# Optimization experiments

Measured on AMD Instinct MI355X. Metric: run time of the kernel, lower is better.

Reference implementation:

```python
import jax, jax.numpy as jnp
import numpy as np

B, S, D, A = 32, 2048, 512, 256


def setup_inputs() -> dict:
    key = jax.random.key(0)
    ks = jax.random.split(key, 9)
    enc = jax.random.normal(ks[0], (B, S, D), dtype=jnp.float32)
    dec = jax.random.normal(ks[1], (B, 1, D), dtype=jnp.float32)
    prev = jax.random.uniform(ks[2], (B, S), dtype=jnp.float32)
    prev = prev / jnp.sum(prev, axis=1, keepdims=True)  # normalized prev attention
    noise = jax.random.normal(ks[3], (B, S), dtype=jnp.float32)
    W = jax.random.normal(ks[4], (A, D), dtype=jnp.float32) / np.sqrt(D)
    V = jax.random.normal(ks[5], (A, D), dtype=jnp.float32) / np.sqrt(D)
    b = jax.random.normal(ks[6], (A,), dtype=jnp.float32)
    v_w = jax.random.normal(ks[7], (1, A), dtype=jnp.float32)
    v_g = jnp.full((1,), np.sqrt(1.0 / A), dtype=jnp.float32)  # weight_norm g init
    v_bias = jax.random.normal(ks[8], (1,), dtype=jnp.float32)
    r = jnp.full((1,), -4.0, dtype=jnp.float32)
    return {"encoder_outputs": enc, "decoder_h": dec, "prev_alpha": prev,
            "noise": noise, "W": W, "V": V, "b": b, "v_w": v_w,
            "v_g": v_g, "v_bias": v_bias, "r": r}


def reference(encoder_outputs, decoder_h, prev_alpha, noise, W, V, b, v_w, v_g, v_bias, r):
    # Energy: tanh-MLP Bahdanau score with weight-normed output projection
    h = jnp.tanh(jnp.einsum('bsd,ad->bsa', encoder_outputs, W)
                 + jnp.einsum('bod,ad->boa', decoder_h, V)  # [B,1,A] broadcasts over S
                 + b)
    w_eff = v_g * v_w / jnp.linalg.norm(v_w)       # weight_norm: g * v / ||v||
    energy = jnp.einsum('bsa,oa->bso', h, w_eff)[..., 0] + v_bias[0] + r[0]  # [B,S]
    # Soft monotonic attention recurrence
    p_select = jax.nn.sigmoid(energy + noise)
    log1mp = jnp.log(jnp.clip(1.0 - p_select, 1e-10, 1.0))
    cumprod_1mp = jnp.exp(jnp.cumsum(log1mp, axis=1))  # safe_cumprod
    alpha = p_select * cumprod_1mp * jnp.cumsum(prev_alpha / cumprod_1mp, axis=1)
    # Context: enc^T @ alpha
    context = jnp.einsum('bsd,bs->bd', encoder_outputs, alpha)
    return context, alpha
```

## Files before the change

### kernel.cpp

```cpp
#include <hip/hip_runtime.h>
#include <math.h>

#define B_  32
#define S_  2048
#define D_  512
#define A_  256
#define BS_ (B_ * S_)

#define WEFF_OFF  0
#define DEC_OFF   256
#define EPART_OFF 8448
#define CTX_OFF   (8448 + BS_)

typedef _Float16 f16x8 __attribute__((ext_vector_type(8)));
typedef __fp16   fp16x2 __attribute__((ext_vector_type(2)));
typedef _Float16 half4 __attribute__((ext_vector_type(4)));
typedef float floatx4 __attribute__((ext_vector_type(4)));

__device__ __forceinline__ void glds16(const void* g, void* l) {
    __builtin_amdgcn_global_load_lds(
        (const __attribute__((address_space(1))) void*)g,
        (__attribute__((address_space(3))) void*)l, 16, 0, 0);
}

__global__ void ma_prep_kernel(const float* __restrict__ v_w,
                               const float* __restrict__ v_g,
                               const float* __restrict__ dec,
                               const float* __restrict__ V,
                               const float* __restrict__ bvec,
                               const float* __restrict__ W,
                               _Float16* __restrict__ W16,
                               float* __restrict__ ws) {
    __shared__ float sh[D_];
    const int bid = blockIdx.x, t = threadIdx.x;
    if (bid == 0) {
        float v = v_w[t];
        float sq = v * v;
        #pragma unroll
        for (int off = 32; off > 0; off >>= 1) sq += __shfl_down(sq, off, 64);
        if ((t & 63) == 0) sh[t >> 6] = sq;
        __syncthreads();
        float n2 = sh[0] + sh[1] + sh[2] + sh[3];
        ws[WEFF_OFF + t] = v_g[0] * v / sqrtf(n2);
    } else if (bid <= B_) {
        const int b = bid - 1;
        sh[t]       = dec[b * D_ + t];
        sh[t + 256] = dec[b * D_ + 256 + t];
        __syncthreads();
        const float4* Vr = (const float4*)(V + (size_t)t * D_);
        float acc = 0.f;
        #pragma unroll 4
        for (int k = 0; k < D_ / 4; ++k) {
            float4 v4 = Vr[k];
            acc = fmaf(v4.x, sh[4*k+0], acc);
            acc = fmaf(v4.y, sh[4*k+1], acc);
            acc = fmaf(v4.z, sh[4*k+2], acc);
            acc = fmaf(v4.w, sh[4*k+3], acc);
        }
        ws[DEC_OFF + b * A_ + t] = acc + bvec[t];
    } else {
        int i = (bid - (B_ + 1)) * 256 + t;
        float4 v = ((const float4*)W)[i];
        half4 h;
        h[0] = (_Float16)v.x; h[1] = (_Float16)v.y;
        h[2] = (_Float16)v.z; h[3] = (_Float16)v.w;
        ((half4*)W16)[i] = h;
    }
}

__global__ __launch_bounds__(512) void ma_energy_mfma(
        const float* __restrict__ enc,
        const _Float16* __restrict__ W16,
        const float* __restrict__ ws_in,
        float* __restrict__ energy) {
    __shared__ __align__(16) float    As[2][128 * 32];
    __shared__ __align__(16) _Float16 Bs[2][256 * 32];
    __shared__ float red[4][128];

    const int t  = threadIdx.x;
    const int bx = blockIdx.x;
    const size_t R0 = (size_t)bx * 128;
    const int batch = bx >> 4;

    const int lane = t & 63, wid = t >> 6;
    const int wm = wid >> 2, wn = wid & 3;
    const int fr = lane & 15, kq = lane >> 4;

    const int arow = t >> 3, ac = t & 7;
    const float* AgS0 = enc + (R0 + (size_t)arow) * D_ + (ac ^ (arow & 7)) * 4;
    const float* AgS1 = AgS0 + (size_t)64 * D_;
    const int brow = t >> 2, bc = t & 3;
    const _Float16* BgS0 = W16 + (size_t)brow * D_ + (bc ^ ((brow >> 1) & 3)) * 8;
    const _Float16* BgS1 = BgS0 + (size_t)128 * D_;

    const int axc0 = ((2 * kq)     ^ (fr & 7)) * 4;
    const int axc1 = ((2 * kq + 1) ^ (fr & 7)) * 4;
    const int bxo  = (kq ^ ((fr >> 1) & 3)) * 8;

    floatx4 acc[4][4];
    #pragma unroll
    for (int m = 0; m < 4; ++m)
        #pragma unroll
        for (int n = 0; n < 4; ++n) acc[m][n] = (floatx4)0.f;

    glds16(AgS0, &As[0][wid * 256]);
    glds16(AgS1, &As[0][wid * 256 + 2048]);
    glds16(BgS0, &Bs[0][wid * 512]);
    glds16(BgS1, &Bs[0][wid * 512 + 4096]);
    __syncthreads();

    #pragma unroll 1
    for (int kt = 0; kt < 16; ++kt) {
        const int cur = kt & 1;
        if (kt < 15) {
            const int nxt = cur ^ 1;
            const int ko = (kt + 1) * 32;
            glds16(AgS0 + ko, &As[nxt][wid * 256]);
            glds16(AgS1 + ko, &As[nxt][wid * 256 + 2048]);
            glds16(BgS0 + ko, &Bs[nxt][wid * 512]);
            glds16(BgS1 + ko, &Bs[nxt][wid * 512 + 4096]);
        }
        f16x8 af[4];
        #pragma unroll
        for (int m = 0; m < 4; ++m) {
            const int rbase = (wm * 64 + m * 16 + fr) * 32;
            float4 lo = *(const float4*)&As[cur][rbase + axc0];
            float4 hi = *(const float4*)&As[cur][rbase + axc1];
            union { fp16x2 h2[4]; f16x8 v; } u;
            u.h2[0] = __builtin_amdgcn_cvt_pkrtz(lo.x, lo.y);
            u.h2[1] = __builtin_amdgcn_cvt_pkrtz(lo.z, lo.w);
            u.h2[2] = __builtin_amdgcn_cvt_pkrtz(hi.x, hi.y);
            u.h2[3] = __builtin_amdgcn_cvt_pkrtz(hi.z, hi.w);
            af[m] = u.v;
        }
        f16x8 bf[4];
        #pragma unroll
        for (int n = 0; n < 4; ++n)
            bf[n] = *(const f16x8*)&Bs[cur][(wn * 64 + n * 16 + fr) * 32 + bxo];
        #pragma unroll
        for (int m = 0; m < 4; ++m)
            #pragma unroll
            for (int n = 0; n < 4; ++n)
                acc[m][n] = __builtin_amdgcn_mfma_f32_16x16x32_f16(af[m], bf[n], acc[m][n], 0, 0, 0);
        __syncthreads();
    }

    const float* weff  = ws_in + WEFF_OFF;
    const float* dterm = ws_in + DEC_OFF + batch * A_;
    float wj[4], dj[4];
    #pragma unroll
    for (int n = 0; n < 4; ++n) {
        int a = wn * 64 + n * 16 + fr;
        wj[n] = weff[a];
        dj[n] = dterm[a];
    }
    #pragma unroll
    for (int m = 0; m < 4; ++m) {
        #pragma unroll
        for (int r = 0; r < 4; ++r) {
            float v = 0.f;
            #pragma unroll
            for (int n = 0; n < 4; ++n) {
                float x = acc[m][n][r] + dj[n];
                float e = __expf(2.f * x);
                v += (1.f - 2.f / (e + 1.f)) * wj[n];
            }
            #pragma unroll
            for (int mask = 1; mask < 16; mask <<= 1)
                v += __shfl_xor(v, mask, 64);
            if (fr == 0)
                red[wn][wm * 64 + m * 16 + (kq << 2) + r] = v;
        }
    }
    __syncthreads();
    if (t < 128)
        energy[R0 + t] = red[0][t] + red[1][t] + red[2][t] + red[3][t];
}

__global__ void ma_scan_kernel(const float* __restrict__ energy,
                               const float* __restrict__ noise,
                               const float* __restrict__ prev,
                               const float* __restrict__ v_bias,
                               const float* __restrict__ r,
                               float* __restrict__ alpha_out) {
    int b = blockIdx.x, t = threadIdx.x;
    const float bias = v_bias[0] + r[0];
    int base = b * S_ + t * 8;
    float p[8], av[8], bv[8];
    #pragma unroll
    for (int i = 0; i < 8; ++i) {
        float e = energy[base + i] + bias + noise[base + i];
        float pi = 1.f / (1.f + expf(-e));
        p[i]  = pi;
        av[i] = fmaxf(1.f - pi, 1e-10f);
        bv[i] = prev[base + i];
    }
    float Ai = 1.f, Bi = 0.f;
    #pragma unroll
    for (int i = 0; i < 8; ++i) { Bi = av[i] * Bi + bv[i]; Ai *= av[i]; }
    int lane = t & 63;
    #pragma unroll
    for (int off = 1; off < 64; off <<= 1) {
        float Ap = __shfl_up(Ai, off, 64);
        float Bp = __shfl_up(Bi, off, 64);
        if (lane >= off) { Bi = Ai * Bp + Bi; Ai = Ai * Ap; }
    }
    __shared__ float wA[4], wB[4];
    int w = t >> 6;
    if (lane == 63) { wA[w] = Ai; wB[w] = Bi; }
    __syncthreads();
    float Ax = __shfl_up(Ai, 1, 64);
    float Bx = __shfl_up(Bi, 1, 64);
    if (lane == 0) { Ax = 1.f; Bx = 0.f; }
    float PwA = 1.f, PwB = 0.f;
    for (int q = 0; q < w; ++q) { PwB = wA[q] * PwB + wB[q]; PwA *= wA[q]; }
    float T = Ax * PwB + Bx;
    #pragma unroll
    for (int i = 0; i < 8; ++i) {
        T = av[i] * T + bv[i];
        alpha_out[base + i] = p[i] * T;
    }
}

__global__ void ma_ctxpart_kernel(const float* __restrict__ enc,
                                  const float* __restrict__ alpha,
                                  float* __restrict__ cpart) {
    int b = blockIdx.x, sc = blockIdx.y, t = threadIdx.x;
    const int sp = t >> 7;
    const int d4 = t & 127;
    const float4* e = (const float4*)(enc + ((size_t)b * S_ + sc * 128) * D_);
    const float* al = alpha + b * S_ + sc * 128;
    float4 acc = {0.f, 0.f, 0.f, 0.f};
    #pragma unroll 4
    for (int s = sp; s < 128; s += 2) {
        float a = al[s];
        float4 v = e[(size_t)s * 128 + d4];
        acc.x = fmaf(v.x, a, acc.x);
        acc.y = fmaf(v.y, a, acc.y);
        acc.z = fmaf(v.z, a, acc.z);
        acc.w = fmaf(v.w, a, acc.w);
    }
    __shared__ float4 sh[128];
    if (sp == 1) sh[d4] = acc;
    __syncthreads();
    if (sp == 0) {
        float4 o = sh[d4];
        acc.x += o.x; acc.y += o.y; acc.z += o.z; acc.w += o.w;
        ((float4*)(cpart + ((size_t)(sc * B_ + b)) * D_))[d4] = acc;
    }
}

__global__ void ma_ctxreduce_kernel(const float* __restrict__ cpart,
                                    float* __restrict__ ctx) {
    int b = blockIdx.x, d = threadIdx.x;
    float s = 0.f;
    #pragma unroll
    for (int q = 0; q < 16; ++q) s += cpart[((size_t)(q * B_ + b)) * D_ + d];
    ctx[b * D_ + d] = s;
}

extern "C" void kernel_launch(void* const* d_in, const int* in_sizes, int n_in,
                              void* d_out, int out_size, void* d_ws, size_t ws_size,
                              hipStream_t stream) {
    const float* enc    = (const float*)d_in[0];
    const float* dec    = (const float*)d_in[1];
    const float* prev   = (const float*)d_in[2];
    const float* noise  = (const float*)d_in[3];
    const float* W      = (const float*)d_in[4];
    const float* V      = (const float*)d_in[5];
    const float* bvec   = (const float*)d_in[6];
    const float* v_w    = (const float*)d_in[7];
    const float* v_g    = (const float*)d_in[8];
    const float* v_bias = (const float*)d_in[9];
    const float* r      = (const float*)d_in[10];

    float* out = (float*)d_out;
    float* ws  = (float*)d_ws;
    float* alpha = out + B_ * D_;
    _Float16* W16 = (_Float16*)(ws + CTX_OFF);

    ma_prep_kernel<<<1 + B_ + 128, 256, 0, stream>>>(v_w, v_g, dec, V, bvec, W, W16, ws);
    ma_energy_mfma<<<512, 512, 0, stream>>>(enc, W16, ws, ws + EPART_OFF);
    ma_scan_kernel<<<B_, 256, 0, stream>>>(ws + EPART_OFF, noise, prev, v_bias, r, alpha);
    dim3 gc(B_, 16);
    ma_ctxpart_kernel<<<gc, 256, 0, stream>>>(enc, alpha, ws + CTX_OFF);
    ma_ctxreduce_kernel<<<B_, 512, 0, stream>>>(ws + CTX_OFF, out);
}
```

Measured before the change: 77.20 us.

## Stage encoder tile through registers and store fp16 in LDS

The encoder A-tile is no longer copied fp32 straight into LDS with global_load_lds. Each thread now loads it into registers, converts it to fp16 once, and writes it to a half-size swizzled LDS buffer after the MFMA loop body. This removes the redundant per-wave fp32->fp16 conversions and halves LDS footprint and A-fragment LDS read traffic. In exchange it adds register pressure and relies on register prefetch latency being hidden behind the MFMAs instead of the async LDS DMA path.

```diff
diff --git a/kernel.cpp b/kernel.cpp
--- a/kernel.cpp
+++ b/kernel.cpp
@@ -73,7 +73,7 @@
         const _Float16* __restrict__ W16,
         const float* __restrict__ ws_in,
         float* __restrict__ energy) {
-    __shared__ __align__(16) float    As[2][128 * 32];
+    __shared__ __align__(16) _Float16 As[2][128 * 32];
     __shared__ __align__(16) _Float16 Bs[2][256 * 32];
     __shared__ float red[4][128];
 
@@ -86,16 +86,15 @@
     const int wm = wid >> 2, wn = wid & 3;
     const int fr = lane & 15, kq = lane >> 4;
 
-    const int arow = t >> 3, ac = t & 7;
-    const float* AgS0 = enc + (R0 + (size_t)arow) * D_ + (ac ^ (arow & 7)) * 4;
-    const float* AgS1 = AgS0 + (size_t)64 * D_;
+    const int ar = t >> 2, aq = t & 3;
+    const float* Ag = enc + (R0 + (size_t)ar) * D_ + aq * 8;
+    const int awc = ((aq ^ ((ar >> 1) & 3)) * 8);
+
     const int brow = t >> 2, bc = t & 3;
     const _Float16* BgS0 = W16 + (size_t)brow * D_ + (bc ^ ((brow >> 1) & 3)) * 8;
     const _Float16* BgS1 = BgS0 + (size_t)128 * D_;
 
-    const int axc0 = ((2 * kq)     ^ (fr & 7)) * 4;
-    const int axc1 = ((2 * kq + 1) ^ (fr & 7)) * 4;
-    const int bxo  = (kq ^ ((fr >> 1) & 3)) * 8;
+    const int fxo = (kq ^ ((fr >> 1) & 3)) * 8;
 
     floatx4 acc[4][4];
     #pragma unroll
@@ -103,47 +102,57 @@
         #pragma unroll
         for (int n = 0; n < 4; ++n) acc[m][n] = (floatx4)0.f;
 
-    glds16(AgS0, &As[0][wid * 256]);
-    glds16(AgS1, &As[0][wid * 256 + 2048]);
-    glds16(BgS0, &Bs[0][wid * 512]);
-    glds16(BgS1, &Bs[0][wid * 512 + 4096]);
+    float4 pa0, pa1;
+
+#define LOADA(kt) do { \
+        pa0 = *(const float4*)(Ag + (kt) * 32); \
+        pa1 = *(const float4*)(Ag + (kt) * 32 + 4); \
+    } while (0)
+
+#define STOREA(buf) do { \
+        union { fp16x2 h2[4]; f16x8 v; } u; \
+        u.h2[0] = __builtin_amdgcn_cvt_pkrtz(pa0.x, pa0.y); \
+        u.h2[1] = __builtin_amdgcn_cvt_pkrtz(pa0.z, pa0.w); \
+        u.h2[2] = __builtin_amdgcn_cvt_pkrtz(pa1.x, pa1.y); \
+        u.h2[3] = __builtin_amdgcn_cvt_pkrtz(pa1.z, pa1.w); \
+        *(f16x8*)&As[buf][ar * 32 + awc] = u.v; \
+    } while (0)
+
+#define STAGEB(kt, buf) do { \
+        glds16(BgS0 + (kt) * 32, &Bs[buf][t * 8]); \
+        glds16(BgS1 + (kt) * 32, &Bs[buf][(512 + t) * 8]); \
+    } while (0)
+
+    STAGEB(0, 0);
+    LOADA(0);
+    STOREA(0);
     __syncthreads();
 
     #pragma unroll 1
     for (int kt = 0; kt < 16; ++kt) {
         const int cur = kt & 1;
         if (kt < 15) {
-            const int nxt = cur ^ 1;
-            const int ko = (kt + 1) * 32;
-            glds16(AgS0 + ko, &As[nxt][wid * 256]);
-            glds16(AgS1 + ko, &As[nxt][wid * 256 + 2048]);
-            glds16(BgS0 + ko, &Bs[nxt][wid * 512]);
-            glds16(BgS1 + ko, &Bs[nxt][wid * 512 + 4096]);
+            STAGEB(kt + 1, cur ^ 1);
+            LOADA(kt + 1);
         }
-        f16x8 af[4];
-        #pragma unroll
-        for (int m = 0; m < 4; ++m) {
-            const int rbase = (wm * 64 + m * 16 + fr) * 32;
-            float4 lo = *(const float4*)&As[cur][rbase + axc0];
-            float4 hi = *(const float4*)&As[cur][rbase + axc1];
-            union { fp16x2 h2[4]; f16x8 v; } u;
-            u.h2[0] = __builtin_amdgcn_cvt_pkrtz(lo.x, lo.y);
-            u.h2[1] = __builtin_amdgcn_cvt_pkrtz(lo.z, lo.w);
-            u.h2[2] = __builtin_amdgcn_cvt_pkrtz(hi.x, hi.y);
-            u.h2[3] = __builtin_amdgcn_cvt_pkrtz(hi.z, hi.w);
-            af[m] = u.v;
-        }
-        f16x8 bf[4];
+        f16x8 af[4], bf[4];
+        #pragma unroll
+        for (int m = 0; m < 4; ++m)
+            af[m] = *(const f16x8*)&As[cur][(wm * 64 + m * 16 + fr) * 32 + fxo];
         #pragma unroll
         for (int n = 0; n < 4; ++n)
-            bf[n] = *(const f16x8*)&Bs[cur][(wn * 64 + n * 16 + fr) * 32 + bxo];
+            bf[n] = *(const f16x8*)&Bs[cur][(wn * 64 + n * 16 + fr) * 32 + fxo];
         #pragma unroll
         for (int m = 0; m < 4; ++m)
             #pragma unroll
             for (int n = 0; n < 4; ++n)
                 acc[m][n] = __builtin_amdgcn_mfma_f32_16x16x32_f16(af[m], bf[n], acc[m][n], 0, 0, 0);
+        if (kt < 15) STOREA(cur ^ 1);
         __syncthreads();
     }
+#undef LOADA
+#undef STOREA
+#undef STAGEB
 
     const float* weff  = ws_in + WEFF_OFF;
     const float* dterm = ws_in + DEC_OFF + batch * A_;
```

Result: slower. 82.01 us (+6.2%).
